# Kernel tuning notes

Hardware: AMD Instinct MI355X
Metric: run time of the kernel (lower is better)

The kernel has to match this reference:

```python
import jax, jax.numpy as jnp
import numpy as np

N_NODES = 100000
N_EDGES = 1600000
IN_F = 128
OUT_F = 64


def setup_inputs() -> dict:
    key = jax.random.key(0)
    k1, k2, k3, k4, k5, k6 = jax.random.split(key, 6)
    stdv = 1.0 / np.sqrt(OUT_F)
    return {
        "input": jax.random.normal(k1, (N_NODES, IN_F), dtype=jnp.float32),
        "weights": jax.random.uniform(k2, (IN_F, OUT_F), minval=-stdv, maxval=stdv, dtype=jnp.float32),
        "bias": jax.random.uniform(k3, (OUT_F,), minval=-stdv, maxval=stdv, dtype=jnp.float32),
        "adj_vals": jax.random.uniform(k4, (N_EDGES,), dtype=jnp.float32),
        "adj_rows": jax.random.randint(k5, (N_EDGES,), 0, N_NODES, dtype=jnp.int32),
        "adj_cols": jax.random.randint(k6, (N_EDGES,), 0, N_NODES, dtype=jnp.int32),
    }


def reference(input, weights, bias, adj_vals, adj_rows, adj_cols):
    # Dense transform: support = input @ W   -> [N, out_features]
    support = jnp.matmul(input, weights)
    # Sparse adjacency matmul (COO SpMM): out[r] += v * support[c]
    msgs = adj_vals[:, None] * support[adj_cols]          # [E, out_features]
    output = jax.ops.segment_sum(msgs, adj_rows, num_segments=N_NODES)
    # Fused bias epilogue
    return output + bias
```

## Files before the change

### kernel.cpp

```cpp
#include <hip/hip_runtime.h>
#include <hip/hip_bf16.h>

#define N_NODES 100000
#define IN_F 128
#define OUT_F 64
#define BROWS 64
#define NB 1563
#define BIN_TILE 4096
#define BCAP 1280
#define OVCAP 131072
#define CSB_CAP 1280

typedef __attribute__((ext_vector_type(8))) short bf16x8;
typedef __attribute__((ext_vector_type(4))) float f32x4;

__device__ __forceinline__ unsigned short f2bf(float x) {
    unsigned u = __float_as_uint(x);
    u += 0x7FFFu + ((u >> 16) & 1u);
    return (unsigned short)(u >> 16);
}
__device__ __forceinline__ float bf2f(unsigned short s) {
    return __uint_as_float(((unsigned)s) << 16);
}

__global__ __launch_bounds__(256) void wt_kernel(
    const float* __restrict__ W, unsigned short* __restrict__ Wt)
{
    int i = blockIdx.x * 256 + threadIdx.x;
    if (i < IN_F * OUT_F) {
        int c = i >> 7, k = i & 127;
        Wt[i] = f2bf(W[k * OUT_F + c]);
    }
}

__global__ __launch_bounds__(256) void gemm_mfma(
    const float* __restrict__ in, const unsigned short* __restrict__ Wt,
    unsigned short* __restrict__ support)
{
    __shared__ unsigned short Dl[64 * 68];
    const int t    = threadIdx.x;
    const int lane = t & 63;
    const int rw   = t >> 6;
    const long rowB = (long)blockIdx.x * 64;
    const long row0 = rowB + rw * 16;

    const int lr = lane & 15;
    const int lk = lane >> 4;

    long arow = row0 + lr;
    if (arow >= N_NODES) arow = N_NODES - 1;
    const float* Ap = in + arow * IN_F + lk * 8;
    const unsigned short* Wp = Wt + lk * 8;

    f32x4 acc0 = {0.f, 0.f, 0.f, 0.f};
    f32x4 acc1 = {0.f, 0.f, 0.f, 0.f};
    f32x4 acc2 = {0.f, 0.f, 0.f, 0.f};
    f32x4 acc3 = {0.f, 0.f, 0.f, 0.f};

    #pragma unroll
    for (int ks = 0; ks < 4; ++ks) {
        const float4 a01 = *(const float4*)(Ap + ks * 32);
        const float4 a23 = *(const float4*)(Ap + ks * 32 + 4);
        bf16x8 af;
        af[0] = (short)f2bf(a01.x); af[1] = (short)f2bf(a01.y);
        af[2] = (short)f2bf(a01.z); af[3] = (short)f2bf(a01.w);
        af[4] = (short)f2bf(a23.x); af[5] = (short)f2bf(a23.y);
        af[6] = (short)f2bf(a23.z); af[7] = (short)f2bf(a23.w);

        const int koff = ks * 32;
        bf16x8 b0 = *(const bf16x8*)(Wp + (0 * 16 + lr) * IN_F + koff);
        bf16x8 b1 = *(const bf16x8*)(Wp + (1 * 16 + lr) * IN_F + koff);
        bf16x8 b2 = *(const bf16x8*)(Wp + (2 * 16 + lr) * IN_F + koff);
        bf16x8 b3 = *(const bf16x8*)(Wp + (3 * 16 + lr) * IN_F + koff);

        acc0 = __builtin_amdgcn_mfma_f32_16x16x32_bf16(af, b0, acc0, 0, 0, 0);
        acc1 = __builtin_amdgcn_mfma_f32_16x16x32_bf16(af, b1, acc1, 0, 0, 0);
        acc2 = __builtin_amdgcn_mfma_f32_16x16x32_bf16(af, b2, acc2, 0, 0, 0);
        acc3 = __builtin_amdgcn_mfma_f32_16x16x32_bf16(af, b3, acc3, 0, 0, 0);
    }

    const int lrow = rw * 16 + lk * 4;
    #pragma unroll
    for (int r = 0; r < 4; ++r) {
        unsigned short* dst = Dl + (lrow + r) * 68;
        dst[ 0 + lr] = f2bf(acc0[r]);
        dst[16 + lr] = f2bf(acc1[r]);
        dst[32 + lr] = f2bf(acc2[r]);
        dst[48 + lr] = f2bf(acc3[r]);
    }
    __syncthreads();

    #pragma unroll
    for (int i = 0; i < 4; ++i) {
        const int idx = t + i * 256;
        const int row = idx >> 4;
        const int c2  = idx & 15;
        const long orow = rowB + row;
        if (orow < N_NODES) {
            const uint2 v = *(const uint2*)(Dl + row * 68 + c2 * 4);
            *(uint2*)(support + orow * OUT_F + c2 * 4) = v;
        }
    }
}

__global__ __launch_bounds__(256) void bin_kernel(
    const int* __restrict__ rows, const int* __restrict__ cols,
    const float* __restrict__ vals, int* __restrict__ cursor,
    int* __restrict__ ovCount, uint4* __restrict__ ovList,
    uint2* __restrict__ binned, int nE)
{
    __shared__ int hist[NB];
    __shared__ int lbase[NB];
    const int t  = threadIdx.x;
    const int tb = blockIdx.x * BIN_TILE;

    for (int i = t; i < NB; i += 256) hist[i] = 0;
    __syncthreads();

    int myr[16], myrank[16];
    #pragma unroll
    for (int i = 0; i < 16; ++i) {
        int e = tb + i * 256 + t;
        if (e < nE) {
            int r = rows[e];
            myr[i] = r;
            myrank[i] = atomicAdd(&hist[r >> 6], 1);
        } else myr[i] = -1;
    }
    __syncthreads();

    for (int i = t; i < NB; i += 256) {
        int h = hist[i];
        lbase[i] = h ? atomicAdd(&cursor[i], h) : 0;
    }
    __syncthreads();

    #pragma unroll
    for (int i = 0; i < 16; ++i) {
        int e = tb + i * 256 + t;
        if (e < nE) {
            const int r = myr[i];
            const int b = r >> 6;
            const int off = lbase[b] + myrank[i];
            if (off < BCAP) {
                unsigned pack = ((unsigned)(r & (BROWS - 1)) << 17)
                              | (unsigned)cols[e];
                binned[(size_t)b * BCAP + off] =
                    make_uint2(pack, __float_as_uint(vals[e]));
            } else {
                int op = atomicAdd(ovCount, 1);
                if (op < OVCAP)
                    ovList[op] = make_uint4((unsigned)r, (unsigned)cols[e],
                                            __float_as_uint(vals[e]), 0u);
            }
        }
    }
}

__global__ __launch_bounds__(1024, 2) void csr_spmm(
    const int* __restrict__ cursor, const uint2* __restrict__ binned,
    const unsigned short* __restrict__ support, const float* __restrict__ bias,
    float* __restrict__ out)
{
    __shared__ uint2 stage[CSB_CAP];
    __shared__ uint2 sorted[CSB_CAP];
    __shared__ int rh[BROWS], rs[BROWS + 1], rc[BROWS];
    const int t = threadIdx.x;
    const int b = blockIdx.x;
    const size_t s = (size_t)b * BCAP;
    const int n = min(cursor[b], BCAP);
    const int wid  = t >> 6;
    const int lane = t & 63;
    const int row0 = b * BROWS;

    if (t < BROWS) rh[t] = 0;
    __syncthreads();

    for (int i = t; i < n; i += 1024) {
        uint2 p = binned[s + i];
        stage[i] = p;
        atomicAdd(&rh[p.x >> 17], 1);
    }
    __syncthreads();
    if (t < BROWS) {
        int v = rh[t];
        int inc = v;
        #pragma unroll
        for (int off = 1; off < BROWS; off <<= 1) {
            int y = __shfl_up(inc, off, 64);
            if (t >= off) inc += y;
        }
        rs[t] = inc - v;
        rc[t] = inc - v;
        if (t == BROWS - 1) rs[BROWS] = inc;
    }
    __syncthreads();
    for (int i = t; i < n; i += 1024) {
        uint2 p = stage[i];
        int pos = atomicAdd(&rc[p.x >> 17], 1);
        sorted[pos] = p;
    }
    __syncthreads();

    #pragma unroll
    for (int q = 0; q < 4; ++q) {
        const int rr = wid * 4 + q;
        const int r  = row0 + rr;
        if (r >= N_NODES) break;
        float acc = bias[lane];
        int j  = rs[rr];
        const int je = rs[rr + 1];
        for (; j + 7 < je; j += 8) {
            uint2 q0 = sorted[j + 0];
            uint2 q1 = sorted[j + 1];
            uint2 q2 = sorted[j + 2];
            uint2 q3 = sorted[j + 3];
            uint2 q4 = sorted[j + 4];
            uint2 q5 = sorted[j + 5];
            uint2 q6 = sorted[j + 6];
            uint2 q7 = sorted[j + 7];
            float g0 = bf2f(support[((size_t)(q0.x & 131071u) << 6) + lane]);
            float g1 = bf2f(support[((size_t)(q1.x & 131071u) << 6) + lane]);
            float g2 = bf2f(support[((size_t)(q2.x & 131071u) << 6) + lane]);
            float g3 = bf2f(support[((size_t)(q3.x & 131071u) << 6) + lane]);
            float g4 = bf2f(support[((size_t)(q4.x & 131071u) << 6) + lane]);
            float g5 = bf2f(support[((size_t)(q5.x & 131071u) << 6) + lane]);
            float g6 = bf2f(support[((size_t)(q6.x & 131071u) << 6) + lane]);
            float g7 = bf2f(support[((size_t)(q7.x & 131071u) << 6) + lane]);
            acc = fmaf(__uint_as_float(q0.y), g0, acc);
            acc = fmaf(__uint_as_float(q1.y), g1, acc);
            acc = fmaf(__uint_as_float(q2.y), g2, acc);
            acc = fmaf(__uint_as_float(q3.y), g3, acc);
            acc = fmaf(__uint_as_float(q4.y), g4, acc);
            acc = fmaf(__uint_as_float(q5.y), g5, acc);
            acc = fmaf(__uint_as_float(q6.y), g6, acc);
            acc = fmaf(__uint_as_float(q7.y), g7, acc);
        }
        for (; j < je; ++j) {
            uint2 p = sorted[j];
            acc = fmaf(__uint_as_float(p.y),
                       bf2f(support[((size_t)(p.x & 131071u) << 6) + lane]),
                       acc);
        }
        out[(size_t)r * OUT_F + lane] = acc;
    }
}

__global__ __launch_bounds__(256) void ovfix_kernel(
    const int* __restrict__ ovCount, const uint4* __restrict__ ovList,
    const unsigned short* __restrict__ support, float* __restrict__ out)
{
    const int n = min(*ovCount, OVCAP);
    const int lane = threadIdx.x & 63;
    for (int e = blockIdx.x * 4 + (threadIdx.x >> 6); e < n; e += 32 * 4) {
        const uint4 p = ovList[e];
        const float m = __uint_as_float(p.z) *
                        bf2f(support[((size_t)p.y << 6) + lane]);
        atomicAdd(&out[((size_t)p.x << 6) + lane], m);
    }
}

__global__ __launch_bounds__(256) void gemm_valu(
    const float* __restrict__ in, const float* __restrict__ W,
    unsigned short* __restrict__ support)
{
    __shared__ float Alds[64 * IN_F];
    const int t = threadIdx.x;
    const long row0 = (long)blockIdx.x * 64;
    #pragma unroll
    for (int i = 0; i < 8; ++i) {
        int fi = t + i * 256;
        int r  = fi >> 5;
        int c4 = (fi & 31) << 2;
        float4 v = make_float4(0.f, 0.f, 0.f, 0.f);
        if (row0 + r < N_NODES)
            v = *(const float4*)(in + (row0 + r) * IN_F + c4);
        *(float4*)(Alds + r * IN_F + c4) = v;
    }
    __syncthreads();
    const int lane = t & 63;
    const int c0   = __builtin_amdgcn_readfirstlane((t >> 6) << 4);
    const float* __restrict__ Wp = W + c0;
    float acc[16];
    #pragma unroll
    for (int i = 0; i < 16; ++i) acc[i] = 0.f;
    const float* Ar = Alds + lane * IN_F;
    for (int k = 0; k < IN_F; ++k) {
        const float a = Ar[k];
        const float4 w0 = *(const float4*)(Wp + k * OUT_F + 0);
        const float4 w1 = *(const float4*)(Wp + k * OUT_F + 4);
        const float4 w2 = *(const float4*)(Wp + k * OUT_F + 8);
        const float4 w3 = *(const float4*)(Wp + k * OUT_F + 12);
        acc[0]  = fmaf(a, w0.x, acc[0]);  acc[1]  = fmaf(a, w0.y, acc[1]);
        acc[2]  = fmaf(a, w0.z, acc[2]);  acc[3]  = fmaf(a, w0.w, acc[3]);
        acc[4]  = fmaf(a, w1.x, acc[4]);  acc[5]  = fmaf(a, w1.y, acc[5]);
        acc[6]  = fmaf(a, w1.z, acc[6]);  acc[7]  = fmaf(a, w1.w, acc[7]);
        acc[8]  = fmaf(a, w2.x, acc[8]);  acc[9]  = fmaf(a, w2.y, acc[9]);
        acc[10] = fmaf(a, w2.z, acc[10]); acc[11] = fmaf(a, w2.w, acc[11]);
        acc[12] = fmaf(a, w3.x, acc[12]); acc[13] = fmaf(a, w3.y, acc[13]);
        acc[14] = fmaf(a, w3.z, acc[14]); acc[15] = fmaf(a, w3.w, acc[15]);
    }
    const long orow = row0 + lane;
    if (orow < N_NODES) {
        unsigned short* o = support + orow * OUT_F + c0;
        #pragma unroll
        for (int i = 0; i < 16; ++i) o[i] = f2bf(acc[i]);
    }
}

__global__ __launch_bounds__(256) void bias_init_kernel(
    float* __restrict__ out, const float* __restrict__ bias, int total4)
{
    const float4* b4 = (const float4*)bias;
    float4* o4 = (float4*)out;
    int i = blockIdx.x * blockDim.x + threadIdx.x;
    int stride = gridDim.x * blockDim.x;
    for (; i < total4; i += stride)
        o4[i] = b4[i & 15];
}

__global__ __launch_bounds__(256) void scatter_kernel(
    const float* __restrict__ vals, const int* __restrict__ rows,
    const int* __restrict__ cols, const unsigned short* __restrict__ support,
    float* __restrict__ out, int nE)
{
    const int e = blockIdx.x * 4 + (threadIdx.x >> 6);
    if (e >= nE) return;
    const int f = threadIdx.x & 63;
    const float m = vals[e] * bf2f(support[(size_t)cols[e] * OUT_F + f]);
    atomicAdd(&out[(size_t)rows[e] * OUT_F + f], m);
}

extern "C" void kernel_launch(void* const* d_in, const int* in_sizes, int n_in,
                              void* d_out, int out_size, void* d_ws, size_t ws_size,
                              hipStream_t stream) {
    const float* input    = (const float*)d_in[0];
    const float* weights  = (const float*)d_in[1];
    const float* bias     = (const float*)d_in[2];
    const float* adj_vals = (const float*)d_in[3];
    const int*   adj_rows = (const int*)d_in[4];
    const int*   adj_cols = (const int*)d_in[5];
    const int nE = in_sizes[3];

    float* out = (float*)d_out;
    const int gemmBlocks = (N_NODES + 63) / 64;
    const int binBlocks  = (nE + BIN_TILE - 1) / BIN_TILE;

    char* ws = (char*)d_ws;
    const size_t off_support = 0;
    const size_t off_wt      = 12800000;
    const size_t off_cursor  = off_wt + 16384;
    const size_t off_binned  = off_cursor + 6272;
    const size_t off_ovlist  = off_binned + (size_t)NB * BCAP * 8;
    const size_t required    = off_ovlist + (size_t)OVCAP * 16;

    unsigned short* support = (unsigned short*)(ws + off_support);
    unsigned short* Wt      = (unsigned short*)(ws + off_wt);
    int*   cursor  = (int*)  (ws + off_cursor);
    uint2* binned  = (uint2*)(ws + off_binned);
    uint4* ovList  = (uint4*)(ws + off_ovlist);
    int*   ovCount = cursor + NB;

    if (ws_size >= required) {
        hipMemsetAsync(cursor, 0, (NB + 1) * sizeof(int), stream);
        hipLaunchKernelGGL(wt_kernel, dim3(32), dim3(256), 0, stream,
                           weights, Wt);
        hipLaunchKernelGGL(gemm_mfma, dim3(gemmBlocks), dim3(256), 0, stream,
                           input, Wt, support);
        hipLaunchKernelGGL(bin_kernel, dim3(binBlocks), dim3(256), 0, stream,
                           adj_rows, adj_cols, adj_vals, cursor,
                           ovCount, ovList, binned, nE);
        hipLaunchKernelGGL(csr_spmm, dim3(NB), dim3(1024), 0, stream,
                           cursor, binned, support, bias, out);
        hipLaunchKernelGGL(ovfix_kernel, dim3(32), dim3(256), 0, stream,
                           ovCount, ovList, support, out);
    } else {
        hipLaunchKernelGGL(gemm_valu, dim3(gemmBlocks), dim3(256), 0, stream,
                           input, weights, support);
        hipLaunchKernelGGL(bias_init_kernel, dim3(2048), dim3(256), 0, stream,
                           out, bias, N_NODES * OUT_F / 4);
        hipLaunchKernelGGL(scatter_kernel, dim3((nE + 3) / 4), dim3(256),
                           0, stream, adj_vals, adj_rows, adj_cols, support,
                           out, nE);
    }
}
```

Baseline: 117.3 us.

## Split per-bin cursors into four segments to cut global atomic contention

The binning kernel now keeps four cursor segments per row bin, chosen by block index, so blocks contend on different global counters. Each bin's storage is split into four fixed-capacity sub-slots, and the SpMM kernel concatenates the segments into shared memory. The binning kernel also moves to 1024-thread blocks with 4 edges per thread. Capacity per segment is smaller, so uneven distribution across segments could push more edges into the overflow path.

```diff
diff --git a/kernel.cpp b/kernel.cpp
--- a/kernel.cpp
+++ b/kernel.cpp
@@ -7,9 +7,11 @@
 #define BROWS 64
 #define NB 1563
 #define BIN_TILE 4096
-#define BCAP 1280
+#define NSEG 4
+#define SCAP 352
+#define BCAP (NSEG * SCAP)
 #define OVCAP 131072
-#define CSB_CAP 1280
+#define CSB_CAP BCAP
 
 typedef __attribute__((ext_vector_type(8))) short bf16x8;
 typedef __attribute__((ext_vector_type(4))) float f32x4;
@@ -103,7 +105,7 @@
     }
 }
 
-__global__ __launch_bounds__(256) void bin_kernel(
+__global__ __launch_bounds__(1024, 2) void bin_kernel(
     const int* __restrict__ rows, const int* __restrict__ cols,
     const float* __restrict__ vals, int* __restrict__ cursor,
     int* __restrict__ ovCount, uint4* __restrict__ ovList,
@@ -113,14 +115,15 @@
     __shared__ int lbase[NB];
     const int t  = threadIdx.x;
     const int tb = blockIdx.x * BIN_TILE;
-
-    for (int i = t; i < NB; i += 256) hist[i] = 0;
-    __syncthreads();
-
-    int myr[16], myrank[16];
-    #pragma unroll
-    for (int i = 0; i < 16; ++i) {
-        int e = tb + i * 256 + t;
+    const int g  = blockIdx.x & (NSEG - 1);
+
+    for (int i = t; i < NB; i += 1024) hist[i] = 0;
+    __syncthreads();
+
+    int myr[4], myrank[4];
+    #pragma unroll
+    for (int i = 0; i < 4; ++i) {
+        int e = tb + i * 1024 + t;
         if (e < nE) {
             int r = rows[e];
             myr[i] = r;
@@ -129,23 +132,23 @@
     }
     __syncthreads();
 
-    for (int i = t; i < NB; i += 256) {
+    for (int i = t; i < NB; i += 1024) {
         int h = hist[i];
-        lbase[i] = h ? atomicAdd(&cursor[i], h) : 0;
-    }
-    __syncthreads();
-
-    #pragma unroll
-    for (int i = 0; i < 16; ++i) {
-        int e = tb + i * 256 + t;
+        lbase[i] = h ? atomicAdd(&cursor[i * NSEG + g], h) : 0;
+    }
+    __syncthreads();
+
+    #pragma unroll
+    for (int i = 0; i < 4; ++i) {
+        int e = tb + i * 1024 + t;
         if (e < nE) {
             const int r = myr[i];
             const int b = r >> 6;
             const int off = lbase[b] + myrank[i];
-            if (off < BCAP) {
+            if (off < SCAP) {
                 unsigned pack = ((unsigned)(r & (BROWS - 1)) << 17)
                               | (unsigned)cols[e];
-                binned[(size_t)b * BCAP + off] =
+                binned[(size_t)b * BCAP + g * SCAP + off] =
                     make_uint2(pack, __float_as_uint(vals[e]));
             } else {
                 int op = atomicAdd(ovCount, 1);
@@ -168,20 +171,38 @@
     const int t = threadIdx.x;
     const int b = blockIdx.x;
     const size_t s = (size_t)b * BCAP;
-    const int n = min(cursor[b], BCAP);
     const int wid  = t >> 6;
     const int lane = t & 63;
     const int row0 = b * BROWS;
 
+    const int n0 = min(cursor[b * NSEG + 0], SCAP);
+    const int n1 = min(cursor[b * NSEG + 1], SCAP);
+    const int n2 = min(cursor[b * NSEG + 2], SCAP);
+    const int n3 = min(cursor[b * NSEG + 3], SCAP);
+    const int o1 = n0, o2 = n0 + n1, o3 = o2 + n2;
+    const int n  = o3 + n3;
+
     if (t < BROWS) rh[t] = 0;
     __syncthreads();
 
-    for (int i = t; i < n; i += 1024) {
-        uint2 p = binned[s + i];
-        stage[i] = p;
-        atomicAdd(&rh[p.x >> 17], 1);
-    }
-    __syncthreads();
+    for (int i = t; i < n0; i += 1024) {
+        uint2 p = binned[s + 0 * SCAP + i];
+        stage[i] = p;           atomicAdd(&rh[p.x >> 17], 1);
+    }
+    for (int i = t; i < n1; i += 1024) {
+        uint2 p = binned[s + 1 * SCAP + i];
+        stage[o1 + i] = p;      atomicAdd(&rh[p.x >> 17], 1);
+    }
+    for (int i = t; i < n2; i += 1024) {
+        uint2 p = binned[s + 2 * SCAP + i];
+        stage[o2 + i] = p;      atomicAdd(&rh[p.x >> 17], 1);
+    }
+    for (int i = t; i < n3; i += 1024) {
+        uint2 p = binned[s + 3 * SCAP + i];
+        stage[o3 + i] = p;      atomicAdd(&rh[p.x >> 17], 1);
+    }
+    __syncthreads();
+
     if (t < BROWS) {
         int v = rh[t];
         int inc = v;
@@ -350,7 +371,7 @@
     const size_t off_support = 0;
     const size_t off_wt      = 12800000;
     const size_t off_cursor  = off_wt + 16384;
-    const size_t off_binned  = off_cursor + 6272;
+    const size_t off_binned  = off_cursor + 25600;
     const size_t off_ovlist  = off_binned + (size_t)NB * BCAP * 8;
     const size_t required    = off_ovlist + (size_t)OVCAP * 16;
 
@@ -359,15 +380,15 @@
     int*   cursor  = (int*)  (ws + off_cursor);
     uint2* binned  = (uint2*)(ws + off_binned);
     uint4* ovList  = (uint4*)(ws + off_ovlist);
-    int*   ovCount = cursor + NB;
+    int*   ovCount = cursor + NB * NSEG;
 
     if (ws_size >= required) {
-        hipMemsetAsync(cursor, 0, (NB + 1) * sizeof(int), stream);
+        hipMemsetAsync(cursor, 0, (NB * NSEG + 1) * sizeof(int), stream);
         hipLaunchKernelGGL(wt_kernel, dim3(32), dim3(256), 0, stream,
                            weights, Wt);
         hipLaunchKernelGGL(gemm_mfma, dim3(gemmBlocks), dim3(256), 0, stream,
                            input, Wt, support);
-        hipLaunchKernelGGL(bin_kernel, dim3(binBlocks), dim3(256), 0, stream,
+        hipLaunchKernelGGL(bin_kernel, dim3(binBlocks), dim3(1024), 0, stream,
                            adj_rows, adj_cols, adj_vals, cursor,
                            ovCount, ovList, binned, nE);
         hipLaunchKernelGGL(csr_spmm, dim3(NB), dim3(1024), 0, stream,
```

Measured after the change: 116.2 us (median of 2 runs). Within noise of the previous version (-0.9%).
